# Optimization experiments

Hardware: AMD Instinct MI355X
Metric: run time of the kernel (lower is better)

Reference implementation:

```python
import jax, jax.numpy as jnp
import numpy as np

D = 1024       # d_model
H = 16         # num_heads
DK = D // H    # head dim (64)
DFF = 4096     # SwiGLU hidden dim
THETA = 10000.0
EPS = 1e-5
B, S = 2, 2048


def setup_inputs() -> dict:
    key = jax.random.key(0)
    ks = jax.random.split(key, 9)
    p = lambda k, shape: jax.random.normal(k, shape, dtype=jnp.float32) * 0.02
    return {
        "x": jax.random.normal(ks[0], (B, S, D), dtype=jnp.float32),
        "w_q": p(ks[1], (D, D)),   # Linear stores [out, in]
        "w_k": p(ks[2], (D, D)),
        "w_v": p(ks[3], (D, D)),
        "w_o": p(ks[4], (D, D)),
        "ln1_w": jnp.ones((D,), dtype=jnp.float32),
        "ln2_w": jnp.ones((D,), dtype=jnp.float32),
        "w1": p(ks[5], (DFF, D)),  # gate-in proj: d_model -> dff
        "w2": p(ks[6], (D, DFF)),  # down proj:    dff -> d_model
        "w3": p(ks[7], (DFF, D)),  # up proj:      d_model -> dff
    }


def _rmsnorm(x, w):
    xf = x.astype(jnp.float32)
    inv = jax.lax.rsqrt(jnp.mean(xf * xf, axis=-1, keepdims=True) + EPS)
    return (inv * xf * w).astype(x.dtype)


def _rope(x, pos):
    # x: [..., seq, DK]; pos: [seq]
    inv_freq = THETA ** (-(jnp.arange(0, DK, 2, dtype=jnp.float32) / DK))  # [DK/2]
    ang = pos.astype(jnp.float32)[:, None] * inv_freq                      # [seq, DK/2]
    cos, sin = jnp.cos(ang), jnp.sin(ang)
    xe, xo = x[..., ::2], x[..., 1::2]
    re = cos * xe - sin * xo
    ro = sin * xe + cos * xo
    return jnp.stack((re, ro), axis=-1).reshape(x.shape)  # interleave even/odd


def reference(x, w_q, w_k, w_v, w_o, ln1_w, ln2_w, w1, w2, w3):
    b, s, d = x.shape
    pos = jnp.arange(s)

    # --- attention sublayer ---
    h = _rmsnorm(x, ln1_w)
    def proj(w):  # [b,s,d] x [d,d] -> [b,H,s,DK]
        return jnp.einsum('bsd,ed->bse', h, w).reshape(b, s, H, DK).transpose(0, 2, 1, 3)
    q = _rope(proj(w_q), pos)
    k = _rope(proj(w_k), pos)
    v = proj(w_v)

    scores = jnp.einsum('bhqd,bhkd->bhqk', q, k) / (DK ** 0.5)
    causal = jnp.tril(jnp.ones((s, s), dtype=bool))
    scores = jnp.where(causal, scores, -jnp.inf)
    attn = jax.nn.softmax(scores, axis=-1)
    o = jnp.einsum('bhqk,bhkd->bhqd', attn, v).transpose(0, 2, 1, 3).reshape(b, s, d)
    x = x + jnp.einsum('bsd,ed->bse', o, w_o)

    # --- SwiGLU FFN sublayer ---
    h2 = _rmsnorm(x, ln2_w)
    u = jnp.einsum('bsd,fd->bsf', h2, w1)
    g = jnp.einsum('bsd,fd->bsf', h2, w3)
    ffn = jnp.einsum('bsf,df->bsd', u * jax.nn.sigmoid(u) * g, w2)
    return x + ffn
```

## Files before the change

### kernel.cpp

```cpp
#include <hip/hip_runtime.h>

typedef _Float16 half_t;
typedef _Float16 f16x8 __attribute__((ext_vector_type(8)));
typedef _Float16 f16x4 __attribute__((ext_vector_type(4)));
typedef _Float16 f16x2 __attribute__((ext_vector_type(2)));
typedef float fx4 __attribute__((ext_vector_type(4)));

typedef __attribute__((address_space(1))) const unsigned int as1_cuint;
typedef __attribute__((address_space(3))) unsigned int as3_uint;

__device__ __forceinline__ void gld16(const void* g, void* l) {
    __builtin_amdgcn_global_load_lds((as1_cuint*)g, (as3_uint*)l, 16, 0, 0);
}

template<int MODE>
__global__ __launch_bounds__(256, 2)
void gemm_bt(const half_t* __restrict__ A,
             const half_t* __restrict__ B0, const half_t* __restrict__ B1,
             const half_t* __restrict__ B2,
             half_t* o0, half_t* o1, half_t* o2, half_t* o3,
             const float* resid, float* outF, half_t* ubuf,
             int M, int N, int K)
{
    __shared__ half_t sA[128 * 32];
    __shared__ half_t sB[128 * 32];
    const int tid = threadIdx.x;
    const int wid = tid >> 6, lane = tid & 63;
    const int lm = lane & 15, lg = lane >> 4;
    const int wr = wid >> 1, wc = wid & 1;
    const int m0 = blockIdx.x * 128, n0 = blockIdx.y * 128;

    const half_t* Bp = B0;
    half_t* outb = o0;
    if (MODE == 1) {
        if (blockIdx.z == 1) { Bp = B1; outb = o1; }
        else if (blockIdx.z == 2) { Bp = B2; outb = o2; }
    }
    if (MODE == 4) {
        if (blockIdx.z == 1) outb = o1;
        else if (blockIdx.z == 2) outb = o2;
        else if (blockIdx.z == 3) outb = o3;
    }

    int Keff = K, koff = 0;
    if (MODE == 4) { Keff = K / gridDim.z; koff = blockIdx.z * Keff; }

    const int srow = tid >> 2;
    const int scolb = (tid & 3) << 4;
    const char* gA = (const char*)(A + (size_t)(m0 + srow) * K + koff) + scolb;
    const char* gB = (const char*)(Bp + (size_t)(n0 + srow) * K + koff) + scolb;
    const size_t rstep = (size_t)64 * K * sizeof(half_t);
    char* lA = (char*)sA + tid * 16;
    char* lB = (char*)sB + tid * 16;

    fx4 acc[4][4] = {};

    for (int kt = 0; kt < Keff; kt += 32) {
        gld16(gA, lA);
        gld16(gA + rstep, lA + 4096);
        gld16(gB, lB);
        gld16(gB + rstep, lB + 4096);
        gA += 64; gB += 64;
        __syncthreads();
        f16x8 aF[4], bF[4];
#pragma unroll
        for (int mi = 0; mi < 4; mi++)
            aF[mi] = *(const f16x8*)(sA + (wr * 64 + mi * 16 + lm) * 32 + lg * 8);
#pragma unroll
        for (int ni = 0; ni < 4; ni++)
            bF[ni] = *(const f16x8*)(sB + (wc * 64 + ni * 16 + lm) * 32 + lg * 8);
#pragma unroll
        for (int mi = 0; mi < 4; mi++)
#pragma unroll
            for (int ni = 0; ni < 4; ni++)
                acc[mi][ni] = __builtin_amdgcn_mfma_f32_16x16x32_f16(aF[mi], bF[ni], acc[mi][ni], 0, 0, 0);
        __syncthreads();
    }

#pragma unroll
    for (int mi = 0; mi < 4; mi++) {
#pragma unroll
        for (int ni = 0; ni < 4; ni++) {
#pragma unroll
            for (int r = 0; r < 4; r++) {
                int m = m0 + wr * 64 + mi * 16 + lg * 4 + r;
                int n = n0 + wc * 64 + ni * 16 + lm;
                float v = acc[mi][ni][r];
                size_t idx = (size_t)m * N + n;
                if (MODE == 0) {
                    outb[idx] = (half_t)v;
                } else if (MODE == 1) {
                    int b = m >> 11, s = m & 2047, hh = n >> 6, dk = n & 63;
                    if (blockIdx.z == 2) {
                        outb[((size_t)(b * 16 + hh) * 64 + dk) * 2048 + s] = (half_t)v;
                    } else {
                        outb[((size_t)(b * 16 + hh) * 2048 + s) * 64 + dk] = (half_t)v;
                    }
                } else if (MODE == 2) {
                    outF[idx] = resid[idx] + v;
                } else if (MODE == 3) {
                    float u = (float)ubuf[idx];
                    float a = u / (1.f + __expf(-u)) * v;
                    ubuf[idx] = (half_t)a;
                } else {
                    outb[idx] = (half_t)v;
                }
            }
        }
    }
}

__global__ __launch_bounds__(256, 8)
void reduce2_k(const float* __restrict__ base,
               const half_t* __restrict__ p0, const half_t* __restrict__ p1,
               float* __restrict__ out, int n4)
{
    int i = blockIdx.x * 256 + threadIdx.x;
    if (i >= n4) return;
    float4 b = ((const float4*)base)[i];
    f16x4 a0 = ((const f16x4*)p0)[i];
    f16x4 a1 = ((const f16x4*)p1)[i];
    float4 o = { b.x + (float)a0[0] + (float)a1[0],
                 b.y + (float)a0[1] + (float)a1[1],
                 b.z + (float)a0[2] + (float)a1[2],
                 b.w + (float)a0[3] + (float)a1[3] };
    ((float4*)out)[i] = o;
}

__global__ __launch_bounds__(256, 8)
void reduce4_k(const half_t* __restrict__ p0, const half_t* __restrict__ p1,
               const half_t* __restrict__ p2, const half_t* __restrict__ p3,
               float* __restrict__ out, int n4)
{
    int i = blockIdx.x * 256 + threadIdx.x;
    if (i >= n4) return;
    float4 b = ((const float4*)out)[i];
    f16x4 a0 = ((const f16x4*)p0)[i];
    f16x4 a1 = ((const f16x4*)p1)[i];
    f16x4 a2 = ((const f16x4*)p2)[i];
    f16x4 a3 = ((const f16x4*)p3)[i];
    float4 o = { b.x + (float)a0[0] + (float)a1[0] + (float)a2[0] + (float)a3[0],
                 b.y + (float)a0[1] + (float)a1[1] + (float)a2[1] + (float)a3[1],
                 b.z + (float)a0[2] + (float)a1[2] + (float)a2[2] + (float)a3[2],
                 b.w + (float)a0[3] + (float)a1[3] + (float)a2[3] + (float)a3[3] };
    ((float4*)out)[i] = o;
}

__global__ __launch_bounds__(256, 4)
void rmsnorm_k(const float* __restrict__ x, const float* __restrict__ w,
               half_t* __restrict__ out)
{
    int row = blockIdx.x * 4 + (threadIdx.x >> 6);
    int lane = threadIdx.x & 63;
    const float4* xr = (const float4*)(x + (size_t)row * 1024);
    float4 v[4];
    float s = 0.f;
#pragma unroll
    for (int i = 0; i < 4; i++) {
        v[i] = xr[lane + 64 * i];
        s += v[i].x * v[i].x + v[i].y * v[i].y + v[i].z * v[i].z + v[i].w * v[i].w;
    }
#pragma unroll
    for (int o = 32; o > 0; o >>= 1) s += __shfl_xor(s, o);
    float inv = rsqrtf(s * (1.f / 1024.f) + 1e-5f);
    const float4* w4 = (const float4*)w;
    f16x4* o4 = (f16x4*)(out + (size_t)row * 1024);
#pragma unroll
    for (int i = 0; i < 4; i++) {
        float4 wv = w4[lane + 64 * i];
        f16x4 ov = { (half_t)(v[i].x * inv * wv.x), (half_t)(v[i].y * inv * wv.y),
                     (half_t)(v[i].z * inv * wv.z), (half_t)(v[i].w * inv * wv.w) };
        o4[lane + 64 * i] = ov;
    }
}

struct CastA { const float* s; half_t* d; int n4; };
struct CastArgs { CastA a[7]; };

__global__ void cast_k(CastArgs ca)
{
    CastA a = ca.a[blockIdx.y];
    int i = blockIdx.x * 256 + threadIdx.x;
    if (i >= a.n4) return;
    float4 v = ((const float4*)a.s)[i];
    ((f16x4*)a.d)[i] = (f16x4){ (half_t)v.x, (half_t)v.y, (half_t)v.z, (half_t)v.w };
}

__global__ void rope_k(half_t* Q, half_t* Kv)
{
    int idx = blockIdx.x * 256 + threadIdx.x;
    half_t* P = blockIdx.y ? Kv : Q;
    float scq = blockIdx.y ? 1.0f : 0.125f;
    int i = idx & 31;
    int s = (idx >> 5) & 2047;
    int bh = idx >> 16;
    float f = __expf((float)i * -0.28782313662f);
    float ang = (float)s * f;
    float c = cosf(ang), sn = sinf(ang);
    f16x2* p = (f16x2*)(P + ((size_t)bh * 2048 + s) * 64 + 2 * i);
    f16x2 xv = *p;
    float xe = (float)xv[0], xo = (float)xv[1];
    *p = (f16x2){ (half_t)((c * xe - sn * xo) * scq), (half_t)((sn * xe + c * xo) * scq) };
}

__global__ __launch_bounds__(256, 2)
void attn_k(const half_t* __restrict__ Q, const half_t* __restrict__ K,
            const half_t* __restrict__ VT, half_t* __restrict__ O)
{
    __shared__ half_t sK[128 * 64];
    __shared__ half_t sVT[64 * 128];
    __shared__ half_t sP[4][16 * 128];
    const int tid = threadIdx.x, wid = tid >> 6, lane = tid & 63;
    const int lm = lane & 15, lg = lane >> 4;
    const int p = blockIdx.x, bh = blockIdx.y;
    const int b = bh >> 4, hh = bh & 15;
    const size_t base = (size_t)bh * (2048 * 64);

    const int krow = tid >> 3;
    const int kcsw = ((tid & 7) ^ (krow & 7)) << 4;
    const int vrow = tid >> 4;
    const int vcsw = ((tid & 15) ^ (vrow & 15)) << 4;
    const char* gK = (const char*)(K + base);
    const char* gV = (const char*)(VT + base);
    char* lK = (char*)sK + tid * 16;
    char* lV = (char*)sVT + tid * 16;
    half_t* sPw = sP[wid];

    f16x8 vone;
#pragma unroll
    for (int j = 0; j < 8; j++) vone[j] = (half_t)1.f;

    for (int ph = 0; ph < 2; ph++) {
        const int qt = ph ? (31 - p) : p;
        const int q0 = qt * 64 + wid * 16;
        const int nT = (qt + 2) >> 1;

        f16x8 bQ[2];
#pragma unroll
        for (int ki = 0; ki < 2; ki++)
            bQ[ki] = *(const f16x8*)(Q + base + (size_t)(q0 + lm) * 64 + ki * 32 + lg * 8);

        fx4 oacc[4] = {};
        fx4 lacc = {};

        for (int t = 0; t < nT; t++) {
            const int kv0 = t * 128;
#pragma unroll
            for (int i = 0; i < 4; i++)
                gld16(gK + (size_t)(kv0 + i * 32 + krow) * 128 + kcsw, lK + i * 4096);
#pragma unroll
            for (int i = 0; i < 4; i++)
                gld16(gV + (size_t)(i * 16 + vrow) * 4096 + (size_t)kv0 * 2 + vcsw, lV + i * 4096);
            __syncthreads();

            fx4 st[8] = {};
#pragma unroll
            for (int ki = 0; ki < 2; ki++) {
#pragma unroll
                for (int mi = 0; mi < 8; mi++) {
                    f16x8 aK = *(const f16x8*)(sK + ((mi * 16 + lm) << 6) +
                                               (((ki * 4 + lg) ^ (lm & 7)) << 3));
                    st[mi] = __builtin_amdgcn_mfma_f32_16x16x32_f16(aK, bQ[ki], st[mi], 0, 0, 0);
                }
            }

            const bool diag = (t == nT - 1);
            const int qg = q0 + lm;
#pragma unroll
            for (int mi = 0; mi < 8; mi++) {
                f16x4 ev;
#pragma unroll
                for (int r = 0; r < 4; r++) {
                    float e = __expf(st[mi][r]);
                    if (diag && (kv0 + mi * 16 + lg * 4 + r > qg)) e = 0.f;
                    ev[r] = (half_t)e;
                }
                *(f16x4*)(sPw + (lm << 7) +
                          ((((mi * 2 + (lg >> 1)) ^ lm) << 3) | ((lg & 1) << 2))) = ev;
            }

#pragma unroll
            for (int k2 = 0; k2 < 4; k2++) {
                f16x8 aP = *(const f16x8*)(sPw + (lm << 7) + (((k2 * 4 + lg) ^ lm) << 3));
#pragma unroll
                for (int ni = 0; ni < 4; ni++) {
                    f16x8 bV = *(const f16x8*)(sVT + ((ni * 16 + lm) << 7) +
                                               (((k2 * 4 + lg) ^ lm) << 3));
                    oacc[ni] = __builtin_amdgcn_mfma_f32_16x16x32_f16(aP, bV, oacc[ni], 0, 0, 0);
                }
                lacc = __builtin_amdgcn_mfma_f32_16x16x32_f16(aP, vone, lacc, 0, 0, 0);
            }
            __syncthreads();
        }

        float inv[4];
#pragma unroll
        for (int r = 0; r < 4; r++) inv[r] = 1.f / lacc[r];
#pragma unroll
        for (int ni = 0; ni < 4; ni++)
#pragma unroll
            for (int r = 0; r < 4; r++) {
                int s = q0 + lg * 4 + r;
                O[((size_t)b * 2048 + s) * 1024 + hh * 64 + ni * 16 + lm] =
                    (half_t)(oacc[ni][r] * inv[r]);
            }
    }
}

extern "C" void kernel_launch(void* const* d_in, const int* in_sizes, int n_in,
                              void* d_out, int out_size, void* d_ws, size_t ws_size,
                              hipStream_t stream)
{
    const float* x   = (const float*)d_in[0];
    const float* wq  = (const float*)d_in[1];
    const float* wk  = (const float*)d_in[2];
    const float* wv  = (const float*)d_in[3];
    const float* wo  = (const float*)d_in[4];
    const float* ln1 = (const float*)d_in[5];
    const float* ln2 = (const float*)d_in[6];
    const float* w1  = (const float*)d_in[7];
    const float* w2  = (const float*)d_in[8];
    const float* w3  = (const float*)d_in[9];

    half_t* W = (half_t*)d_ws;
    const size_t Mi = 1048576;
    half_t* wq16 = W;
    half_t* wk16 = W + Mi;
    half_t* wv16 = W + 2 * Mi;
    half_t* wo16 = W + 3 * Mi;
    half_t* w116 = W + 4 * Mi;
    half_t* w316 = W + 8 * Mi;
    half_t* w216 = W + 12 * Mi;
    half_t* h16  = W + 16 * Mi;
    half_t* q16  = W + 20 * Mi;
    half_t* k16  = W + 24 * Mi;
    half_t* vt16 = W + 28 * Mi;
    half_t* u16  = W + 16 * Mi;
    half_t* h216 = W + 32 * Mi;
    half_t* P0   = W + 20 * Mi;
    half_t* P1   = W + 24 * Mi;
    half_t* D0   = W;
    half_t* D1   = W + 4 * Mi;
    half_t* D2   = W + 8 * Mi;
    half_t* D3   = W + 36 * Mi;

    CastArgs ca;
    ca.a[0] = { wq, wq16, 262144 };
    ca.a[1] = { wk, wk16, 262144 };
    ca.a[2] = { wv, wv16, 262144 };
    ca.a[3] = { wo, wo16, 262144 };
    ca.a[4] = { w1, w116, 1048576 };
    ca.a[5] = { w2, w216, 1048576 };
    ca.a[6] = { w3, w316, 1048576 };

    cast_k<<<dim3(4096, 7), 256, 0, stream>>>(ca);
    rmsnorm_k<<<dim3(1024), 256, 0, stream>>>(x, ln1, h16);
    gemm_bt<1><<<dim3(32, 8, 3), 256, 0, stream>>>(h16, wq16, wk16, wv16,
                                                   q16, k16, vt16, nullptr,
                                                   nullptr, nullptr, nullptr, 4096, 1024, 1024);
    rope_k<<<dim3(8192, 2), 256, 0, stream>>>(q16, k16);
    attn_k<<<dim3(16, 32), 256, 0, stream>>>(q16, k16, vt16, h16);
    gemm_bt<4><<<dim3(32, 8, 2), 256, 0, stream>>>(h16, wo16, nullptr, nullptr,
                                                   P0, P1, nullptr, nullptr,
                                                   nullptr, nullptr, nullptr,
                                                   4096, 1024, 1024);
    reduce2_k<<<dim3(4096), 256, 0, stream>>>(x, P0, P1, (float*)d_out, 1048576);
    rmsnorm_k<<<dim3(1024), 256, 0, stream>>>((const float*)d_out, ln2, h216);
    gemm_bt<0><<<dim3(32, 32, 1), 256, 0, stream>>>(h216, w116, nullptr, nullptr,
                                                    u16, nullptr, nullptr, nullptr,
                                                    nullptr, nullptr, nullptr, 4096, 4096, 1024);
    gemm_bt<3><<<dim3(32, 32, 1), 256, 0, stream>>>(h216, w316, nullptr, nullptr,
                                                    nullptr, nullptr, nullptr, nullptr,
                                                    nullptr, nullptr, u16, 4096, 4096, 1024);
    gemm_bt<4><<<dim3(32, 8, 4), 256, 0, stream>>>(u16, w216, nullptr, nullptr,
                                                   D0, D1, D2, D3,
                                                   nullptr, nullptr, nullptr,
                                                   4096, 1024, 4096);
    reduce4_k<<<dim3(4096), 256, 0, stream>>>(D0, D1, D2, D3, (float*)d_out, 1048576);
    (void)in_sizes; (void)n_in; (void)out_size; (void)ws_size;
}
```

Measured before the change: 415.6 us.

## Fuse gate/up GEMMs into dual-B kernel and merge residual add with RMSNorm

Replaces the separate w1 and w3 GEMMs (the second one reading back u to apply SiLU*g) with a single kernel. It loads the A tile once, accumulates both products, and writes the SwiGLU activation directly. It also merges the attention-output partial-sum reduction with the second RMSNorm into one row kernel that writes both the fp32 residual and the fp16 normalized input. This removes a launch, one full read of h2, the u round trip through memory, and a separate pass over the residual, at the cost of doubled accumulator registers in the dual GEMM, which may lower occupancy or cause spills.

```diff
diff --git a/kernel.cpp b/kernel.cpp
--- a/kernel.cpp
+++ b/kernel.cpp
@@ -19,7 +19,6 @@
              const half_t* __restrict__ B0, const half_t* __restrict__ B1,
              const half_t* __restrict__ B2,
              half_t* o0, half_t* o1, half_t* o2, half_t* o3,
-             const float* resid, float* outF, half_t* ubuf,
              int M, int N, int K)
 {
     __shared__ half_t sA[128 * 32];
@@ -87,21 +86,13 @@
                 int n = n0 + wc * 64 + ni * 16 + lm;
                 float v = acc[mi][ni][r];
                 size_t idx = (size_t)m * N + n;
-                if (MODE == 0) {
-                    outb[idx] = (half_t)v;
-                } else if (MODE == 1) {
+                if (MODE == 1) {
                     int b = m >> 11, s = m & 2047, hh = n >> 6, dk = n & 63;
                     if (blockIdx.z == 2) {
                         outb[((size_t)(b * 16 + hh) * 64 + dk) * 2048 + s] = (half_t)v;
                     } else {
                         outb[((size_t)(b * 16 + hh) * 2048 + s) * 64 + dk] = (half_t)v;
                     }
-                } else if (MODE == 2) {
-                    outF[idx] = resid[idx] + v;
-                } else if (MODE == 3) {
-                    float u = (float)ubuf[idx];
-                    float a = u / (1.f + __expf(-u)) * v;
-                    ubuf[idx] = (half_t)a;
                 } else {
                     outb[idx] = (half_t)v;
                 }
@@ -110,21 +101,115 @@
     }
 }
 
-__global__ __launch_bounds__(256, 8)
-void reduce2_k(const float* __restrict__ base,
+__global__ __launch_bounds__(256, 2)
+void gemm_dual(const half_t* __restrict__ A,
+               const half_t* __restrict__ B1, const half_t* __restrict__ B2,
+               half_t* __restrict__ out, int M, int N, int K)
+{
+    __shared__ half_t sA[128 * 32];
+    __shared__ half_t sB1[128 * 32];
+    __shared__ half_t sB2[128 * 32];
+    const int tid = threadIdx.x;
+    const int wid = tid >> 6, lane = tid & 63;
+    const int lm = lane & 15, lg = lane >> 4;
+    const int wr = wid >> 1, wc = wid & 1;
+    const int m0 = blockIdx.x * 128, n0 = blockIdx.y * 128;
+
+    const int srow = tid >> 2;
+    const int scolb = (tid & 3) << 4;
+    const char* gA = (const char*)(A + (size_t)(m0 + srow) * K) + scolb;
+    const char* gB1 = (const char*)(B1 + (size_t)(n0 + srow) * K) + scolb;
+    const char* gB2 = (const char*)(B2 + (size_t)(n0 + srow) * K) + scolb;
+    const size_t rstep = (size_t)64 * K * sizeof(half_t);
+    char* lA = (char*)sA + tid * 16;
+    char* lB1 = (char*)sB1 + tid * 16;
+    char* lB2 = (char*)sB2 + tid * 16;
+
+    fx4 accU[4][4] = {};
+    fx4 accG[4][4] = {};
+
+    for (int kt = 0; kt < K; kt += 32) {
+        gld16(gA, lA);
+        gld16(gA + rstep, lA + 4096);
+        gld16(gB1, lB1);
+        gld16(gB1 + rstep, lB1 + 4096);
+        gld16(gB2, lB2);
+        gld16(gB2 + rstep, lB2 + 4096);
+        gA += 64; gB1 += 64; gB2 += 64;
+        __syncthreads();
+        f16x8 aF[4], b1F[4], b2F[4];
+#pragma unroll
+        for (int mi = 0; mi < 4; mi++)
+            aF[mi] = *(const f16x8*)(sA + (wr * 64 + mi * 16 + lm) * 32 + lg * 8);
+#pragma unroll
+        for (int ni = 0; ni < 4; ni++) {
+            b1F[ni] = *(const f16x8*)(sB1 + (wc * 64 + ni * 16 + lm) * 32 + lg * 8);
+            b2F[ni] = *(const f16x8*)(sB2 + (wc * 64 + ni * 16 + lm) * 32 + lg * 8);
+        }
+#pragma unroll
+        for (int mi = 0; mi < 4; mi++)
+#pragma unroll
+            for (int ni = 0; ni < 4; ni++) {
+                accU[mi][ni] = __builtin_amdgcn_mfma_f32_16x16x32_f16(aF[mi], b1F[ni], accU[mi][ni], 0, 0, 0);
+                accG[mi][ni] = __builtin_amdgcn_mfma_f32_16x16x32_f16(aF[mi], b2F[ni], accG[mi][ni], 0, 0, 0);
+            }
+        __syncthreads();
+    }
+
+#pragma unroll
+    for (int mi = 0; mi < 4; mi++) {
+#pragma unroll
+        for (int ni = 0; ni < 4; ni++) {
+#pragma unroll
+            for (int r = 0; r < 4; r++) {
+                int m = m0 + wr * 64 + mi * 16 + lg * 4 + r;
+                int n = n0 + wc * 64 + ni * 16 + lm;
+                float u = accU[mi][ni][r];
+                float g = accG[mi][ni][r];
+                out[(size_t)m * N + n] = (half_t)(u / (1.f + __expf(-u)) * g);
+            }
+        }
+    }
+}
+
+__global__ __launch_bounds__(256, 4)
+void addnorm_k(const float* __restrict__ x,
                const half_t* __restrict__ p0, const half_t* __restrict__ p1,
-               float* __restrict__ out, int n4)
-{
-    int i = blockIdx.x * 256 + threadIdx.x;
-    if (i >= n4) return;
-    float4 b = ((const float4*)base)[i];
-    f16x4 a0 = ((const f16x4*)p0)[i];
-    f16x4 a1 = ((const f16x4*)p1)[i];
-    float4 o = { b.x + (float)a0[0] + (float)a1[0],
-                 b.y + (float)a0[1] + (float)a1[1],
-                 b.z + (float)a0[2] + (float)a1[2],
-                 b.w + (float)a0[3] + (float)a1[3] };
-    ((float4*)out)[i] = o;
+               const float* __restrict__ w,
+               float* __restrict__ outF, half_t* __restrict__ outH)
+{
+    int row = blockIdx.x * 4 + (threadIdx.x >> 6);
+    int lane = threadIdx.x & 63;
+    const float4* xr = (const float4*)(x + (size_t)row * 1024);
+    const f16x4* p0r = (const f16x4*)(p0 + (size_t)row * 1024);
+    const f16x4* p1r = (const f16x4*)(p1 + (size_t)row * 1024);
+    float4 v[4];
+    float s = 0.f;
+#pragma unroll
+    for (int i = 0; i < 4; i++) {
+        float4 xv = xr[lane + 64 * i];
+        f16x4 a0 = p0r[lane + 64 * i];
+        f16x4 a1 = p1r[lane + 64 * i];
+        v[i].x = xv.x + (float)a0[0] + (float)a1[0];
+        v[i].y = xv.y + (float)a0[1] + (float)a1[1];
+        v[i].z = xv.z + (float)a0[2] + (float)a1[2];
+        v[i].w = xv.w + (float)a0[3] + (float)a1[3];
+        s += v[i].x * v[i].x + v[i].y * v[i].y + v[i].z * v[i].z + v[i].w * v[i].w;
+    }
+#pragma unroll
+    for (int o = 32; o > 0; o >>= 1) s += __shfl_xor(s, o);
+    float inv = rsqrtf(s * (1.f / 1024.f) + 1e-5f);
+    const float4* w4 = (const float4*)w;
+    float4* oF = (float4*)(outF + (size_t)row * 1024);
+    f16x4* oH = (f16x4*)(outH + (size_t)row * 1024);
+#pragma unroll
+    for (int i = 0; i < 4; i++) {
+        oF[lane + 64 * i] = v[i];
+        float4 wv = w4[lane + 64 * i];
+        f16x4 ov = { (half_t)(v[i].x * inv * wv.x), (half_t)(v[i].y * inv * wv.y),
+                     (half_t)(v[i].z * inv * wv.z), (half_t)(v[i].w * inv * wv.w) };
+        oH[lane + 64 * i] = ov;
+    }
 }
 
 __global__ __launch_bounds__(256, 8)
@@ -335,7 +420,7 @@
     half_t* q16  = W + 20 * Mi;
     half_t* k16  = W + 24 * Mi;
     half_t* vt16 = W + 28 * Mi;
-    half_t* u16  = W + 16 * Mi;
+    half_t* a16  = W + 16 * Mi;
     half_t* h216 = W + 32 * Mi;
     half_t* P0   = W + 20 * Mi;
     half_t* P1   = W + 24 * Mi;
@@ -357,24 +442,18 @@
     rmsnorm_k<<<dim3(1024), 256, 0, stream>>>(x, ln1, h16);
     gemm_bt<1><<<dim3(32, 8, 3), 256, 0, stream>>>(h16, wq16, wk16, wv16,
                                                    q16, k16, vt16, nullptr,
-                                                   nullptr, nullptr, nullptr, 4096, 1024, 1024);
+                                                   4096, 1024, 1024);
     rope_k<<<dim3(8192, 2), 256, 0, stream>>>(q16, k16);
     attn_k<<<dim3(16, 32), 256, 0, stream>>>(q16, k16, vt16, h16);
     gemm_bt<4><<<dim3(32, 8, 2), 256, 0, stream>>>(h16, wo16, nullptr, nullptr,
                                                    P0, P1, nullptr, nullptr,
-                                                   nullptr, nullptr, nullptr,
                                                    4096, 1024, 1024);
-    reduce2_k<<<dim3(4096), 256, 0, stream>>>(x, P0, P1, (float*)d_out, 1048576);
-    rmsnorm_k<<<dim3(1024), 256, 0, stream>>>((const float*)d_out, ln2, h216);
-    gemm_bt<0><<<dim3(32, 32, 1), 256, 0, stream>>>(h216, w116, nullptr, nullptr,
-                                                    u16, nullptr, nullptr, nullptr,
-                                                    nullptr, nullptr, nullptr, 4096, 4096, 1024);
-    gemm_bt<3><<<dim3(32, 32, 1), 256, 0, stream>>>(h216, w316, nullptr, nullptr,
-                                                    nullptr, nullptr, nullptr, nullptr,
-                                                    nullptr, nullptr, u16, 4096, 4096, 1024);
-    gemm_bt<4><<<dim3(32, 8, 4), 256, 0, stream>>>(u16, w216, nullptr, nullptr,
+    addnorm_k<<<dim3(1024), 256, 0, stream>>>(x, P0, P1, ln2,
+                                              (float*)d_out, h216);
+    gemm_dual<<<dim3(32, 32), 256, 0, stream>>>(h216, w116, w316, a16,
+                                                4096, 4096, 1024);
+    gemm_bt<4><<<dim3(32, 8, 4), 256, 0, stream>>>(a16, w216, nullptr, nullptr,
                                                    D0, D1, D2, D3,
-                                                   nullptr, nullptr, nullptr,
                                                    4096, 1024, 4096);
     reduce4_k<<<dim3(4096), 256, 0, stream>>>(D0, D1, D2, D3, (float*)d_out, 1048576);
     (void)in_sizes; (void)n_in; (void)out_size; (void)ws_size;
```

Measured after the change: 387.5 us. 6.7% less time.
